# Kernel tuning notes

Hardware: AMD Instinct MI355X
Metric: run time of the kernel (lower is better)

Reference implementation:

```python
import jax, jax.numpy as jnp
import numpy as np

B, IN, U = 16, 1024, 1024


def _wSw(W, S):
    # W: [i,u], S: [b,i,i] -> W^T S W : [b,u,u]
    return jnp.einsum('iu,bij,jv->buv', W, S, W)


def _xSx(x, Wsig):
    # (sum_i x_i^2) * W_Sigma, broadcast over batch
    return jnp.sum(x * x, axis=1)[:, None, None] * Wsig


def _trS(S, Wsig):
    return jnp.trace(S, axis1=1, axis2=2)[:, None, None] * Wsig


def _hadamard_sigma(s1, s2, m1, m2):
    # s1*s2 + diag(m1) s2 diag(m1) + diag(m2) s1 diag(m2)
    return (s1 * s2
            + m1[:, :, None] * s2 * m1[:, None, :]
            + m2[:, :, None] * s1 * m2[:, None, :])


def _act_sigma(g, S):
    # S * outer(g, g)
    return S * (g[:, :, None] * g[:, None, :])


def setup_inputs() -> dict:
    key = jax.random.key(0)
    ks = jax.random.split(key, 16)
    f32 = jnp.float32
    init_mu, ini_sigma = 0.05, -4.6
    inp = {
        'mu_inputs': jax.random.normal(ks[0], (B, IN), f32),
        'sigma_inputs': 0.01 * jax.random.normal(ks[1], (B, IN, IN), f32),
        'prev_state': 0.1 * jax.random.normal(ks[2], (B, U), f32),
        'Sigma_state': 0.01 * jax.random.normal(ks[3], (B, U, U), f32),
        'U_z': init_mu * jax.random.normal(ks[4], (IN, U), f32),
        'uz_sigma': jnp.full((U,), ini_sigma, f32),
        'W_z': init_mu * jax.random.normal(ks[5], (U, U), f32),
        'wz_sigma': jnp.full((U,), ini_sigma, f32),
        'U_r': init_mu * jax.random.normal(ks[6], (IN, U), f32),
        'ur_sigma': jnp.full((U,), ini_sigma, f32),
        'W_r': init_mu * jax.random.normal(ks[7], (U, U), f32),
        'wr_sigma': jnp.full((U,), ini_sigma, f32),
        'U_h': init_mu * jax.random.normal(ks[8], (IN, U), f32),
        'uh_sigma': jnp.full((U,), ini_sigma, f32),
        'W_h': init_mu * jax.random.normal(ks[9], (U, U), f32),
        'wh_sigma': jnp.full((U,), ini_sigma, f32),
    }
    return inp


def reference(mu_inputs, sigma_inputs, prev_state, Sigma_state,
              U_z, uz_sigma, W_z, wz_sigma,
              U_r, ur_sigma, W_r, wr_sigma,
              U_h, uh_sigma, W_h, wh_sigma):
    sp = jax.nn.softplus
    # ---- z gate ----
    pre_z = mu_inputs @ U_z + prev_state @ W_z
    z = jax.nn.sigmoid(pre_z)
    Uz_S, Wz_S = jnp.diag(sp(uz_sigma)), jnp.diag(sp(wz_sigma))
    Sigma_zz = (_wSw(U_z, sigma_inputs) + _xSx(mu_inputs, Uz_S) + _trS(sigma_inputs, Uz_S)
                + _wSw(W_z, Sigma_state) + _xSx(prev_state, Wz_S) + _trS(Sigma_state, Wz_S))
    Sigma_z = _act_sigma(z * (1.0 - z), Sigma_zz)  # analytic d sigmoid
    # ---- r gate ----
    pre_r = mu_inputs @ U_r + prev_state @ W_r
    r = jax.nn.sigmoid(pre_r)
    Ur_S, Wr_S = jnp.diag(sp(ur_sigma)), jnp.diag(sp(wr_sigma))
    Sigma_rr = (_wSw(U_r, sigma_inputs) + _xSx(mu_inputs, Ur_S) + _trS(sigma_inputs, Ur_S)
                + _wSw(W_r, Sigma_state) + _xSx(prev_state, Wr_S) + _trS(Sigma_state, Wr_S))
    Sigma_r = _act_sigma(r * (1.0 - r), Sigma_rr)
    # ---- h gate ----
    sr = prev_state * r
    pre_h = mu_inputs @ U_h + sr @ W_h
    h = jnp.tanh(pre_h)
    Uh_S, Wh_S = jnp.diag(sp(uh_sigma)), jnp.diag(sp(wh_sigma))
    sigma_g = _hadamard_sigma(Sigma_state, Sigma_r, prev_state, r)
    Sigma_hh = (_wSw(U_h, sigma_inputs) + _xSx(mu_inputs, Uh_S) + _trS(sigma_inputs, Uh_S)
                + _wSw(W_h, sigma_g) + _xSx(sr, Wh_S) + _trS(sigma_g, Wh_S))
    Sigma_h = _act_sigma(1.0 - h * h, Sigma_hh)  # analytic d tanh
    # ---- combine ----
    mu_out = z * prev_state + (1.0 - z) * h
    sigma_a = _hadamard_sigma(Sigma_z, Sigma_state, z, prev_state)
    sigma_b = _hadamard_sigma(Sigma_z, Sigma_h, 1.0 - z, h)
    sigma_ab = Sigma_z * (prev_state[:, :, None] * h[:, None, :])
    sigma_abT = Sigma_z * (h[:, :, None] * prev_state[:, None, :])
    Sigma_out = sigma_a + sigma_b - sigma_ab - sigma_abT
    Sigma_out = jnp.where(jnp.isfinite(Sigma_out), Sigma_out, jnp.zeros_like(Sigma_out))
    eye = jnp.eye(Sigma_out.shape[-1], dtype=bool)
    Sigma_out = jnp.where(eye, jnp.abs(Sigma_out), Sigma_out)
    return mu_out, Sigma_out
```

## Files before the change

### kernel.cpp

```cpp
#include <hip/hip_runtime.h>
#include <math.h>


#define B_  16
#define N_  1024
#define NN_ (1024*1024)

typedef __bf16 bf16x8 __attribute__((ext_vector_type(8)));
typedef float  f32x4  __attribute__((ext_vector_type(4)));
typedef unsigned short ushort8v __attribute__((ext_vector_type(8)));

__device__ __forceinline__ unsigned short f2bf(float f) {
  union { float f; unsigned int u; } v; v.f = f;
  unsigned int r = v.u + 0x7fffu + ((v.u >> 16) & 1u);
  return (unsigned short)(r >> 16);
}
__device__ __forceinline__ float bf2f(unsigned short h) {
  union { unsigned int u; float f; } v; v.u = ((unsigned int)h) << 16;
  return v.f;
}
__device__ __forceinline__ float f4get(const float4& v, int q) {
  return q == 0 ? v.x : (q == 1 ? v.y : (q == 2 ? v.z : v.w));
}
__device__ __forceinline__ unsigned short u4get(const ushort4& v, int q) {
  return q == 0 ? v.x : (q == 1 ? v.y : (q == 2 ? v.z : v.w));
}

__device__ __forceinline__ void gload_lds16(const void* g, void* l) {
  __builtin_amdgcn_global_load_lds((__attribute__((address_space(1))) void*)g,
                                   (__attribute__((address_space(3))) void*)l,
                                   16, 0, 0);
}

#define MFMA_ __builtin_amdgcn_mfma_f32_16x16x32_bf16
#define SBAR_()  do { __builtin_amdgcn_sched_barrier(0); \
                      __builtin_amdgcn_s_barrier(); \
                      __builtin_amdgcn_sched_barrier(0); } while (0)

template<int OMODE, int PAIR>
__global__ __launch_bounds__(512)
void gemm8p(const unsigned short* __restrict__ A, int lda, long aStride, int koffA,
            const unsigned short* __restrict__ Bm, const unsigned short* __restrict__ Bm2,
            int ldb, long bStride, int K,
            void* __restrict__ Out, int ldo, long oStride, int noff,
            const float* __restrict__ act,
            const float* __restrict__ spU, const float* __restrict__ spW,
            const float* __restrict__ dU, const float* __restrict__ dW,
            const unsigned short* __restrict__ SzP, const float* __restrict__ SstP,
            const float* __restrict__ zV, const float* __restrict__ prevV,
            const float* __restrict__ hV)
{
  __shared__ __align__(16) char ldsb[131072];
  const int id = blockIdx.x;
  const int xcd = id & 7, rest = id >> 3;
  const int mt = rest & 3, pp = rest >> 2;
  const int panel = xcd + (pp << 3);
  const int nt = panel & 3;
  const int b  = (panel >> 2) & 15;
  const int ps = PAIR ? (panel >> 6) : 0;
  const unsigned short* Bsel = (PAIR && ps) ? Bm2 : Bm;
  const int kofx = koffA + (ps ? 1024 : 0);
  const int nofx = noff  + (ps ? 1024 : 0);
  const int mbase = mt << 8, nbase = nt << 8;
  const int tid = threadIdx.x, lane = tid & 63, w = tid >> 6;
  const int wm = w >> 2, wn = w & 3;
  const int NT = K >> 6;

  f32x4 acc[8][4];
  const f32x4 zero4 = {0.f, 0.f, 0.f, 0.f};
#pragma unroll
  for (int i = 0; i < 8; i++)
#pragma unroll
    for (int j = 0; j < 4; j++) acc[i][j] = zero4;

  const int l3 = lane >> 3, l7 = lane & 7;
  const int posg = l7 ^ l3;
  const int gr = (l3 << 1) + (posg >> 2);
  const int gc = (posg & 3) << 3;
  const int bi0 = w << 1, bi1 = bi0 + 1;
  const int rS0 = ((bi0 >> 1) << 4) + gr, cS0 = ((bi0 & 1) << 5) + gc;
  const int rS1 = ((bi1 >> 1) << 4) + gr, cS1 = ((bi1 & 1) << 5) + gc;
  const unsigned short* Ab = A + (size_t)b * aStride + (size_t)mbase * lda + kofx;
  const unsigned short* Bb = Bsel + (size_t)b * bStride + (size_t)nbase * ldb;
  const int d0 = w << 11, d1 = (w << 11) + 1024;

  auto SA = [&](int tt, int h) {
    char* dst = ldsb + ((tt & 1) << 16) + (h << 14);
    const unsigned short* s = Ab + (size_t)(h << 7) * lda + ((size_t)tt << 6);
    gload_lds16(s + (size_t)rS0 * lda + cS0, dst + d0);
    gload_lds16(s + (size_t)rS1 * lda + cS1, dst + d1);
  };
  auto SB = [&](int tt, int h) {
    char* dst = ldsb + ((tt & 1) << 16) + 32768 + (h << 14);
    const unsigned short* s = Bb + (size_t)(h << 7) * ldb + ((size_t)tt << 6);
    gload_lds16(s + (size_t)rS0 * ldb + cS0, dst + d0);
    gload_lds16(s + (size_t)rS1 * ldb + cS1, dst + d1);
  };

  const int lrow = lane & 15, c4 = lane >> 4;
  const int aoff = ((lrow >> 1) << 7) + (((((lrow & 1) << 2) | c4) ^ (lrow >> 1)) << 4);
  const int abase = wm << 14;
  const int bbase = 32768 + ((wn >> 1) << 14);
  const int brg   = (wn & 1) << 2;
  auto LDA = [&](const char* pb, int mi, int ks) -> bf16x8 {
    return *(const bf16x8*)(pb + abase + (((mi << 1) + ks) << 10) + aoff);
  };
  auto LDB = [&](const char* pb, int ni, int ks) -> bf16x8 {
    return *(const bf16x8*)(pb + bbase + ((((brg + ni) << 1) + ks) << 10) + aoff);
  };

  SA(0, 0); SA(0, 1); SB(0, 0); SB(0, 1);
  if (NT > 1) { SB(1, 0); SB(1, 1); }
  asm volatile("s_waitcnt vmcnt(4)" ::: "memory");
  SBAR_();

  bf16x8 avA[4], avB[4], bvA[4], bvB[4];
#pragma unroll
  for (int i = 0; i < 4; i++) avB[i] = LDA(ldsb, i, 0);
#pragma unroll
  for (int i = 0; i < 4; i++) bvB[i] = LDB(ldsb, i, 0);
  __builtin_amdgcn_sched_barrier(0);

  for (int kt = 0; kt < NT; ++kt) {
    const char* pb = ldsb + ((kt & 1) << 16);
    const char* pn = ldsb + (((kt + 1) & 1) << 16);
#pragma unroll
    for (int i = 0; i < 4; i++) avA[i] = LDA(pb, 4 + i, 0);
    if (kt + 1 < NT) SA(kt + 1, 0);
    SBAR_();
    __builtin_amdgcn_s_setprio(1);
#pragma unroll
    for (int ni = 0; ni < 4; ni++)
#pragma unroll
      for (int mi = 0; mi < 4; mi++)
        acc[mi][ni] = MFMA_(avB[mi], bvB[ni], acc[mi][ni], 0, 0, 0);
    __builtin_amdgcn_s_setprio(0);
    SBAR_();
#pragma unroll
    for (int i = 0; i < 4; i++) avB[i] = LDA(pb, i, 1);
#pragma unroll
    for (int i = 0; i < 4; i++) bvA[i] = LDB(pb, i, 1);
    if (kt + 1 < NT) SA(kt + 1, 1);
    SBAR_();
    __builtin_amdgcn_s_setprio(1);
#pragma unroll
    for (int ni = 0; ni < 4; ni++)
#pragma unroll
      for (int mi = 0; mi < 4; mi++)
        acc[4 + mi][ni] = MFMA_(avA[mi], bvB[ni], acc[4 + mi][ni], 0, 0, 0);
    __builtin_amdgcn_s_setprio(0);
    SBAR_();
#pragma unroll
    for (int i = 0; i < 4; i++) avA[i] = LDA(pb, 4 + i, 1);
    SBAR_();
    __builtin_amdgcn_s_setprio(1);
#pragma unroll
    for (int ni = 0; ni < 4; ni++)
#pragma unroll
      for (int mi = 0; mi < 4; mi++)
        acc[mi][ni] = MFMA_(avB[mi], bvA[ni], acc[mi][ni], 0, 0, 0);
    __builtin_amdgcn_s_setprio(0);
    SBAR_();
    if (kt + 2 < NT) {
      SB(kt + 2, 0); SB(kt + 2, 1);
      asm volatile("s_waitcnt vmcnt(4)" ::: "memory");
    } else if (kt + 1 < NT) {
      asm volatile("s_waitcnt vmcnt(0)" ::: "memory");
    }
    SBAR_();
    if (kt + 1 < NT) {
#pragma unroll
      for (int i = 0; i < 4; i++) avB[i] = LDA(pn, i, 0);
#pragma unroll
      for (int i = 0; i < 4; i++) bvB[i] = LDB(pn, i, 0);
    }
    __builtin_amdgcn_sched_barrier(0);
    __builtin_amdgcn_s_setprio(1);
#pragma unroll
    for (int ni = 0; ni < 4; ni++)
#pragma unroll
      for (int mi = 0; mi < 4; mi++)
        acc[4 + mi][ni] = MFMA_(avA[mi], bvA[ni], acc[4 + mi][ni], 0, 0, 0);
    __builtin_amdgcn_s_setprio(0);
    SBAR_();
  }

  if (OMODE == 2) {
    const float* ghb = act + b * N_;
    const float dUb = dU[b], dWb = dW[b];
    const float* zb = zV + b * N_;
    const float* pv = prevV + b * N_;
    const float* hb = hV + b * N_;
    const unsigned short* SzB = SzP + (size_t)b * NN_;
    const float* SstB = SstP + (size_t)b * NN_;
    float zvv[4], pvv[4], hvv[4], gvv[4];
    int vcol[4];
#pragma unroll
    for (int ni = 0; ni < 4; ni++) {
      const int v = nbase + wn * 64 + ni * 16 + (lane & 15);
      vcol[ni] = v;
      zvv[ni] = zb[v]; pvv[ni] = pv[v]; hvv[ni] = hb[v]; gvv[ni] = ghb[v];
    }
#pragma unroll
    for (int mi = 0; mi < 8; mi++) {
      const int u0 = mbase + wm * 128 + mi * 16 + ((lane >> 4) << 2);
#pragma unroll
      for (int r = 0; r < 4; r++) {
        const int u = u0 + r;
        const float zu = zb[u], pu = pv[u], hu = hb[u], gu = ghb[u];
        const float diag = dUb * spU[u] + dWb * spW[u];
#pragma unroll
        for (int ni = 0; ni < 4; ni++) {
          const int v = vcol[ni];
          float shh = acc[mi][ni][r];
          if (u == v) shh += diag;
          shh *= gu * gvv[ni];
          const float szv = bf2f(SzB[(size_t)u * N_ + v]);
          const float stt = SstB[(size_t)u * N_ + v];
          float res = szv * stt + zu * zvv[ni] * stt + pu * pvv[ni] * szv
                    + szv * shh + (1.f - zu) * (1.f - zvv[ni]) * shh + hu * hvv[ni] * szv
                    - szv * (pu * hvv[ni]) - szv * (hu * pvv[ni]);
          if (!isfinite(res)) res = 0.f;
          if (u == v) res = fabsf(res);
          ((float*)Out)[(size_t)b * oStride + (size_t)u * ldo + v] = res;
        }
      }
    }
  } else {
    __syncthreads();
    unsigned short* scr = (unsigned short*)(ldsb + w * 16384);
    const float* actb = (OMODE == 1) ? (act + b * N_) : nullptr;
    float dUb = 0.f, dWb = 0.f;
    if (OMODE == 1) { dUb = dU[b]; dWb = dW[b]; }
#pragma unroll
    for (int mi = 0; mi < 8; mi++) {
      const int rl0 = mi * 16 + ((lane >> 4) << 2);
#pragma unroll
      for (int ni = 0; ni < 4; ni++) {
        const int cl = ni * 16 + (lane & 15);
#pragma unroll
        for (int r = 0; r < 4; r++) {
          const int rl = rl0 + r;
          float val = acc[mi][ni][r];
          if (OMODE == 1) {
            const int u = mbase + wm * 128 + rl, v = nbase + wn * 64 + cl;
            if (u == v) val += dUb * spU[u] + dWb * spW[u];
            val *= actb[u] * actb[v];
          }
          scr[rl * 64 + ((((cl >> 3) ^ (rl & 7))) << 3) + (cl & 7)] = f2bf(val);
        }
      }
    }
    asm volatile("s_waitcnt lgkmcnt(0)" ::: "memory");
    __builtin_amdgcn_sched_barrier(0);
    unsigned short* ob = (unsigned short*)Out + (size_t)b * oStride
        + (size_t)(mbase + wm * 128) * ldo + nofx + nbase + wn * 64;
#pragma unroll
    for (int pq = 0; pq < 16; pq++) {
      const int row = pq * 8 + (lane >> 3);
      const int ch = (lane & 7) ^ (row & 7);
      ushort8v vv = *(const ushort8v*)&scr[row * 64 + ((lane & 7) << 3)];
      *(ushort8v*)(ob + (size_t)row * ldo + ch * 8) = vv;
    }
  }
}


__global__ void conv_bf16_2(const float* __restrict__ in0, unsigned short* __restrict__ out0,
                            const float* __restrict__ in1, unsigned short* __restrict__ out1,
                            int n4)
{
  const float* in = blockIdx.y ? in1 : in0;
  unsigned short* out = blockIdx.y ? out1 : out0;
  int i = blockIdx.x * 256 + threadIdx.x;
  const int stride = gridDim.x * 256;
  for (; i < n4; i += stride) {
    const float4 v = ((const float4*)in)[i];
    ushort4 o;
    o.x = f2bf(v.x); o.y = f2bf(v.y); o.z = f2bf(v.z); o.w = f2bf(v.w);
    ((ushort4*)out)[i] = o;
  }
}

__global__ void build_AT(const float* __restrict__ Uz, const float* __restrict__ Wz,
                         const float* __restrict__ Ur, const float* __restrict__ Wr,
                         const float* __restrict__ Uh, const float* __restrict__ Wh,
                         unsigned short* __restrict__ AT)
{
  __shared__ float tile[32][33];
  const int g = blockIdx.z;
  const float* U = g == 0 ? Uz : (g == 1 ? Ur : Uh);
  const float* W = g == 0 ? Wz : (g == 1 ? Wr : Wh);
  const int u0  = blockIdx.x * 32;
  const int k0g = blockIdx.y * 32;
  const float* src = (k0g >= 1024) ? W : U;
  const int kloc = k0g & 1023;
  const int tx = threadIdx.x & 31, ty = threadIdx.x >> 5;
  unsigned short* out = AT + (size_t)g * N_ * 2048;
#pragma unroll
  for (int i = 0; i < 32; i += 8) tile[ty + i][tx] = src[(size_t)(kloc + ty + i) * N_ + u0 + tx];
  __syncthreads();
#pragma unroll
  for (int i = 0; i < 32; i += 8)
    out[(size_t)(u0 + ty + i) * 2048 + k0g + tx] = f2bf(tile[tx][ty + i]);
}

__global__ void softplus6(const float* a0, const float* a1, const float* a2,
                          const float* a3, const float* a4, const float* a5,
                          float* __restrict__ sp)
{
  const float* src[6] = {a0, a1, a2, a3, a4, a5};
  const int g = blockIdx.x;
  const float* s = src[g];
  for (int i = threadIdx.x; i < N_; i += 256) {
    float x = s[i];
    sp[g * N_ + i] = (x > 20.f) ? x : log1pf(expf(x));
  }
}

__global__ void scalars1(const float* __restrict__ mu, const float* __restrict__ prev,
                         const float* __restrict__ sin_, const float* __restrict__ Sst,
                         float* __restrict__ dA, float* __restrict__ dBzr)
{
  __shared__ float red[256];
  const int b = blockIdx.x;
  float s1 = 0.f, s2 = 0.f;
  for (int i = threadIdx.x; i < N_; i += 256) {
    const float m = mu[b * N_ + i];
    s1 += m * m + sin_[(size_t)b * NN_ + (size_t)i * (N_ + 1)];
    const float p = prev[b * N_ + i];
    s2 += p * p + Sst[(size_t)b * NN_ + (size_t)i * (N_ + 1)];
  }
  red[threadIdx.x] = s1; __syncthreads();
  for (int s = 128; s > 0; s >>= 1) { if (threadIdx.x < s) red[threadIdx.x] += red[threadIdx.x + s]; __syncthreads(); }
  if (threadIdx.x == 0) dA[b] = red[0];
  __syncthreads();
  red[threadIdx.x] = s2; __syncthreads();
  for (int s = 128; s > 0; s >>= 1) { if (threadIdx.x < s) red[threadIdx.x] += red[threadIdx.x + s]; __syncthreads(); }
  if (threadIdx.x == 0) dBzr[b] = red[0];
}

__global__ __launch_bounds__(256)
void gate_pre2(const float* __restrict__ x1, const float* __restrict__ x2,
               const float* __restrict__ U0, const float* __restrict__ W0,
               const float* __restrict__ U1, const float* __restrict__ W1,
               float* __restrict__ Ppart)
{
  const int g  = blockIdx.z;
  const int ks = blockIdx.y;
  const int out = blockIdx.x * 256 + threadIdx.x;
  const int b = out >> 10, col = out & 1023;
  const float* x = (ks < 4) ? x1 : x2;
  const float* Wm = (g == 0) ? ((ks < 4) ? U0 : W0) : ((ks < 4) ? U1 : W1);
  const int k0 = (ks & 3) * 256;
  const float* xb = x + b * N_ + k0;
  const float* wp = Wm + (size_t)k0 * N_ + col;
  float acc = 0.f;
#pragma unroll 8
  for (int k = 0; k < 256; k++)
    acc += xb[k] * wp[(size_t)k * N_];
  Ppart[(g * 8 + ks) * (B_ * N_) + out] = acc;
}

__global__ void gate_act2(const float* __restrict__ P,
                          float* __restrict__ z, float* __restrict__ gz,
                          float* __restrict__ r, float* __restrict__ gr)
{
  const int out = blockIdx.x * 256 + threadIdx.x;
  float a0 = 0.f, a1 = 0.f;
#pragma unroll
  for (int ks = 0; ks < 8; ks++) {
    a0 += P[ks * (B_ * N_) + out];
    a1 += P[(8 + ks) * (B_ * N_) + out];
  }
  const float s0 = 1.f / (1.f + expf(-a0));
  const float s1 = 1.f / (1.f + expf(-a1));
  z[out] = s0; gz[out] = s0 * (1.f - s0);
  r[out] = s1; gr[out] = s1 * (1.f - s1);
}

__global__ __launch_bounds__(256)
void gate_pre1(const float* __restrict__ x1, const float* __restrict__ x2,
               const float* __restrict__ U0, const float* __restrict__ W0,
               float* __restrict__ Ppart)
{
  const int ks = blockIdx.y;
  const int out = blockIdx.x * 256 + threadIdx.x;
  const int b = out >> 10, col = out & 1023;
  const float* x = (ks < 4) ? x1 : x2;
  const float* Wm = (ks < 4) ? U0 : W0;
  const int k0 = (ks & 3) * 256;
  const float* xb = x + b * N_ + k0;
  const float* wp = Wm + (size_t)k0 * N_ + col;
  float acc = 0.f;
#pragma unroll 8
  for (int k = 0; k < 256; k++)
    acc += xb[k] * wp[(size_t)k * N_];
  Ppart[ks * (B_ * N_) + out] = acc;
}

__global__ void gate_act1(const float* __restrict__ P,
                          const float* __restrict__ z, const float* __restrict__ prev,
                          float* __restrict__ h, float* __restrict__ gh,
                          float* __restrict__ mu_out)
{
  const int out = blockIdx.x * 256 + threadIdx.x;
  float a0 = 0.f;
#pragma unroll
  for (int ks = 0; ks < 8; ks++) a0 += P[ks * (B_ * N_) + out];
  const float s = tanhf(a0);
  h[out] = s; gh[out] = 1.f - s * s;
  const float zz = z[out];
  mu_out[out] = zz * prev[out] + (1.f - zz) * s;
}

__global__ void sr_csr(const float* __restrict__ prev, const float* __restrict__ r,
                       float* __restrict__ sr, float* __restrict__ csr)
{
  __shared__ float red[256];
  const int b = blockIdx.x;
  float s = 0.f;
  for (int i = threadIdx.x; i < N_; i += 256) {
    const float v = prev[b * N_ + i] * r[b * N_ + i];
    sr[b * N_ + i] = v;
    s += v * v;
  }
  red[threadIdx.x] = s; __syncthreads();
  for (int k = 128; k > 0; k >>= 1) { if (threadIdx.x < k) red[threadIdx.x] += red[threadIdx.x + k]; __syncthreads(); }
  if (threadIdx.x == 0) csr[b] = red[0];
}

__global__ void hadamard_sg(const unsigned short* __restrict__ SstH,
                            unsigned short* __restrict__ Sg,
                            const float* __restrict__ prev, const float* __restrict__ r)
{
  const size_t idx = ((size_t)blockIdx.x * 256 + threadIdx.x) * 4;
  const int b = (int)(idx >> 20);
  const int rem = (int)(idx & (NN_ - 1));
  const int i = rem >> 10, j0 = rem & 1023;
  const float pi = prev[b * N_ + i], ri = r[b * N_ + i];
  const ushort4 ss4 = *(const ushort4*)(SstH + (size_t)b * NN_ + rem);
  const ushort4 sr4 = *(const ushort4*)(Sg + (size_t)b * NN_ + rem);
  ushort4 o;
  unsigned short* op = (unsigned short*)&o;
#pragma unroll
  for (int q = 0; q < 4; q++) {
    const float srv = bf2f(u4get(sr4, q));
    const float stv = bf2f(u4get(ss4, q));
    const float pj = prev[b * N_ + j0 + q];
    const float rj = r[b * N_ + j0 + q];
    op[q] = f2bf(stv * srv + pi * pj * srv + ri * rj * stv);
  }
  *(ushort4*)(Sg + (size_t)b * NN_ + rem) = o;
}

__global__ void scalars2(const unsigned short* __restrict__ Sg,
                         const float* __restrict__ csr, float* __restrict__ dBh)
{
  __shared__ float red[256];
  const int b = blockIdx.x;
  float s = 0.f;
  for (int i = threadIdx.x; i < N_; i += 256)
    s += bf2f(Sg[(size_t)b * NN_ + (size_t)i * (N_ + 1)]);
  red[threadIdx.x] = s; __syncthreads();
  for (int k = 128; k > 0; k >>= 1) { if (threadIdx.x < k) red[threadIdx.x] += red[threadIdx.x + k]; __syncthreads(); }
  if (threadIdx.x == 0) dBh[b] = red[0] + csr[b];
}


extern "C" void kernel_launch(void* const* d_in, const int* in_sizes, int n_in,
                              void* d_out, int out_size, void* d_ws, size_t ws_size,
                              hipStream_t stream)
{
  const float* mu   = (const float*)d_in[0];
  const float* sin_ = (const float*)d_in[1];
  const float* prev = (const float*)d_in[2];
  const float* Sst  = (const float*)d_in[3];
  const float* Uz = (const float*)d_in[4];  const float* uzs = (const float*)d_in[5];
  const float* Wz = (const float*)d_in[6];  const float* wzs = (const float*)d_in[7];
  const float* Ur = (const float*)d_in[8];  const float* urs = (const float*)d_in[9];
  const float* Wr = (const float*)d_in[10]; const float* wrs = (const float*)d_in[11];
  const float* Uh = (const float*)d_in[12]; const float* uhs = (const float*)d_in[13];
  const float* Wh = (const float*)d_in[14]; const float* whs = (const float*)d_in[15];

  char* ws = (char*)d_ws;
  size_t off = 0;
  auto take = [&](size_t bytes) -> char* {
    char* p = ws + off;
    off = (off + bytes + 255) & ~(size_t)255;
    return p;
  };
  unsigned short* Tcm = (unsigned short*)take((size_t)B_ * 2048 * 1024 * 2);
  unsigned short* Sz  = (unsigned short*)take((size_t)B_ * NN_ * 2);
  unsigned short* Sg  = (unsigned short*)take((size_t)B_ * NN_ * 2);
  unsigned short* AT  = (unsigned short*)take((size_t)3 * N_ * 2048 * 2);
  float* Ppart = (float*)take((size_t)16 * B_ * N_ * 4);
  float* sp   = (float*)take(6 * N_ * 4);
  float* z    = (float*)take(B_ * N_ * 4);
  float* gz   = (float*)take(B_ * N_ * 4);
  float* rr   = (float*)take(B_ * N_ * 4);
  float* gr   = (float*)take(B_ * N_ * 4);
  float* h    = (float*)take(B_ * N_ * 4);
  float* gh   = (float*)take(B_ * N_ * 4);
  float* sr   = (float*)take(B_ * N_ * 4);
  float* dA   = (float*)take(64);
  float* dBzr = (float*)take(64);
  float* dBh  = (float*)take(64);
  float* csr  = (float*)take(64);
  if (off > ws_size) return;

  float* mu_out = (float*)d_out;
  float* SigOut = (float*)d_out + (size_t)B_ * N_;
  unsigned short* SinH = (unsigned short*)SigOut;
  unsigned short* SstH = (unsigned short*)SigOut + (size_t)B_ * NN_;

  const unsigned short* ATz = AT;
  const unsigned short* ATr = AT + (size_t)N_ * 2048;
  const unsigned short* ATh = AT + (size_t)2 * N_ * 2048;

  conv_bf16_2<<<dim3(2048, 2), 256, 0, stream>>>(sin_, SinH, Sst, SstH, B_ * NN_ / 4);
  softplus6<<<6, 256, 0, stream>>>(uzs, wzs, urs, wrs, uhs, whs, sp);
  scalars1<<<16, 256, 0, stream>>>(mu, prev, sin_, Sst, dA, dBzr);
  build_AT<<<dim3(32, 64, 3), 256, 0, stream>>>(Uz, Wz, Ur, Wr, Uh, Wh, AT);
  gate_pre2<<<dim3(64, 8, 2), 256, 0, stream>>>(mu, prev, Uz, Wz, Ur, Wr, Ppart);
  gate_act2<<<64, 256, 0, stream>>>(Ppart, z, gz, rr, gr);
  sr_csr<<<16, 256, 0, stream>>>(prev, rr, sr, csr);
  gate_pre1<<<dim3(64, 8), 256, 0, stream>>>(mu, sr, Uh, Wh, Ppart);
  gate_act1<<<64, 256, 0, stream>>>(Ppart, z, prev, h, gh, mu_out);

  const long tS = (long)2048 * 1024;

  gemm8p<0, 1><<<512, 512, 0, stream>>>(ATz, 2048, 0, 0, SinH, SstH, 1024, (long)NN_, 1024,
                                        Tcm, 2048, tS, 0, nullptr, nullptr, nullptr, nullptr, nullptr,
                                        nullptr, nullptr, nullptr, nullptr, nullptr);
  gemm8p<1, 0><<<256, 512, 0, stream>>>(ATz, 2048, 0, 0, Tcm, nullptr, 2048, tS, 2048,
                                        Sz, 1024, (long)NN_, 0, gz, sp + 0, sp + 1024, dA, dBzr,
                                        nullptr, nullptr, nullptr, nullptr, nullptr);
  gemm8p<0, 1><<<512, 512, 0, stream>>>(ATr, 2048, 0, 0, SinH, SstH, 1024, (long)NN_, 1024,
                                        Tcm, 2048, tS, 0, nullptr, nullptr, nullptr, nullptr, nullptr,
                                        nullptr, nullptr, nullptr, nullptr, nullptr);
  gemm8p<1, 0><<<256, 512, 0, stream>>>(ATr, 2048, 0, 0, Tcm, nullptr, 2048, tS, 2048,
                                        Sg, 1024, (long)NN_, 0, gr, sp + 2048, sp + 3072, dA, dBzr,
                                        nullptr, nullptr, nullptr, nullptr, nullptr);
  hadamard_sg<<<16384, 256, 0, stream>>>(SstH, Sg, prev, rr);
  scalars2<<<16, 256, 0, stream>>>(Sg, csr, dBh);
  gemm8p<0, 1><<<512, 512, 0, stream>>>(ATh, 2048, 0, 0, SinH, Sg, 1024, (long)NN_, 1024,
                                        Tcm, 2048, tS, 0, nullptr, nullptr, nullptr, nullptr, nullptr,
                                        nullptr, nullptr, nullptr, nullptr, nullptr);
  gemm8p<2, 0><<<256, 512, 0, stream>>>(ATh, 2048, 0, 0, Tcm, nullptr, 2048, tS, 2048,
                                        SigOut, 1024, (long)NN_, 0, gh, sp + 4096, sp + 5120, dA, dBh,
                                        Sz, Sst, z, prev, h);
}
```

Baseline: 547.8 us.

## Fuse Hadamard sigma_g into r-gate GEMM epilogue and vectorize final epilogue

Adds an OMODE 3 epilogue to the second-stage r-gate GEMM that applies the Hadamard combination with Sigma_state, prev and r directly before writing Sg. This removes the separate hadamard_sg kernel and its extra read and write pass over a 16x1024x1024 bf16 tensor. The OMODE 2 final epilogue is also moved to go through the LDS swizzle, so it does 8-wide vector loads and stores instead of strided scalar accesses. In exchange the Sigma_hh accumulator is now rounded to bf16 before the final combine, which adds precision loss.

```diff
diff --git a/kernel.cpp b/kernel.cpp
--- a/kernel.cpp
+++ b/kernel.cpp
@@ -18,12 +18,6 @@
 __device__ __forceinline__ float bf2f(unsigned short h) {
   union { unsigned int u; float f; } v; v.u = ((unsigned int)h) << 16;
   return v.f;
-}
-__device__ __forceinline__ float f4get(const float4& v, int q) {
-  return q == 0 ? v.x : (q == 1 ? v.y : (q == 2 ? v.z : v.w));
-}
-__device__ __forceinline__ unsigned short u4get(const ushort4& v, int q) {
-  return q == 0 ? v.x : (q == 1 ? v.y : (q == 2 ? v.z : v.w));
 }
 
 __device__ __forceinline__ void gload_lds16(const void* g, void* l) {
@@ -185,82 +179,98 @@
     SBAR_();
   }
 
-  if (OMODE == 2) {
-    const float* ghb = act + b * N_;
-    const float dUb = dU[b], dWb = dW[b];
-    const float* zb = zV + b * N_;
-    const float* pv = prevV + b * N_;
-    const float* hb = hV + b * N_;
-    const unsigned short* SzB = SzP + (size_t)b * NN_;
-    const float* SstB = SstP + (size_t)b * NN_;
-    float zvv[4], pvv[4], hvv[4], gvv[4];
-    int vcol[4];
+  __syncthreads();
+  unsigned short* scr = (unsigned short*)(ldsb + w * 16384);
+  const float* actb = act ? (act + b * N_) : nullptr;
+  float dUb = 0.f, dWb = 0.f;
+  if (OMODE != 0) { dUb = dU[b]; dWb = dW[b]; }
+
+#pragma unroll
+  for (int mi = 0; mi < 8; mi++) {
+    const int rl0 = mi * 16 + ((lane >> 4) << 2);
 #pragma unroll
     for (int ni = 0; ni < 4; ni++) {
-      const int v = nbase + wn * 64 + ni * 16 + (lane & 15);
-      vcol[ni] = v;
-      zvv[ni] = zb[v]; pvv[ni] = pv[v]; hvv[ni] = hb[v]; gvv[ni] = ghb[v];
-    }
-#pragma unroll
-    for (int mi = 0; mi < 8; mi++) {
-      const int u0 = mbase + wm * 128 + mi * 16 + ((lane >> 4) << 2);
+      const int cl = ni * 16 + (lane & 15);
 #pragma unroll
       for (int r = 0; r < 4; r++) {
-        const int u = u0 + r;
-        const float zu = zb[u], pu = pv[u], hu = hb[u], gu = ghb[u];
-        const float diag = dUb * spU[u] + dWb * spW[u];
-#pragma unroll
-        for (int ni = 0; ni < 4; ni++) {
-          const int v = vcol[ni];
-          float shh = acc[mi][ni][r];
-          if (u == v) shh += diag;
-          shh *= gu * gvv[ni];
-          const float szv = bf2f(SzB[(size_t)u * N_ + v]);
-          const float stt = SstB[(size_t)u * N_ + v];
-          float res = szv * stt + zu * zvv[ni] * stt + pu * pvv[ni] * szv
-                    + szv * shh + (1.f - zu) * (1.f - zvv[ni]) * shh + hu * hvv[ni] * szv
-                    - szv * (pu * hvv[ni]) - szv * (hu * pvv[ni]);
-          if (!isfinite(res)) res = 0.f;
-          if (u == v) res = fabsf(res);
-          ((float*)Out)[(size_t)b * oStride + (size_t)u * ldo + v] = res;
+        const int rl = rl0 + r;
+        float val = acc[mi][ni][r];
+        if (OMODE != 0) {
+          const int u = mbase + wm * 128 + rl, v = nbase + wn * 64 + cl;
+          if (u == v) val += dUb * spU[u] + dWb * spW[u];
+          val *= actb[u] * actb[v];
         }
+        scr[rl * 64 + ((((cl >> 3) ^ (rl & 7))) << 3) + (cl & 7)] = f2bf(val);
       }
     }
-  } else {
-    __syncthreads();
-    unsigned short* scr = (unsigned short*)(ldsb + w * 16384);
-    const float* actb = (OMODE == 1) ? (act + b * N_) : nullptr;
-    float dUb = 0.f, dWb = 0.f;
-    if (OMODE == 1) { dUb = dU[b]; dWb = dW[b]; }
-#pragma unroll
-    for (int mi = 0; mi < 8; mi++) {
-      const int rl0 = mi * 16 + ((lane >> 4) << 2);
-#pragma unroll
-      for (int ni = 0; ni < 4; ni++) {
-        const int cl = ni * 16 + (lane & 15);
-#pragma unroll
-        for (int r = 0; r < 4; r++) {
-          const int rl = rl0 + r;
-          float val = acc[mi][ni][r];
-          if (OMODE == 1) {
-            const int u = mbase + wm * 128 + rl, v = nbase + wn * 64 + cl;
-            if (u == v) val += dUb * spU[u] + dWb * spW[u];
-            val *= actb[u] * actb[v];
-          }
-          scr[rl * 64 + ((((cl >> 3) ^ (rl & 7))) << 3) + (cl & 7)] = f2bf(val);
-        }
+  }
+  asm volatile("s_waitcnt lgkmcnt(0)" ::: "memory");
+  __builtin_amdgcn_sched_barrier(0);
+
+#pragma unroll
+  for (int pq = 0; pq < 16; pq++) {
+    const int row = pq * 8 + (lane >> 3);
+    const int slot = lane & 7;
+    const int ch = slot ^ (row & 7);
+    const int u = mbase + wm * 128 + row;
+    const int v0 = nbase + wn * 64 + (ch << 3);
+    ushort8v s8 = *(const ushort8v*)&scr[row * 64 + (slot << 3)];
+    if (OMODE == 0 || OMODE == 1) {
+      unsigned short* ob = (unsigned short*)Out + (size_t)b * oStride
+                         + (size_t)u * ldo + nofx + v0;
+      *(ushort8v*)ob = s8;
+    } else if (OMODE == 3) {
+      const float pu = prevV[b * N_ + u];
+      const float ru = zV[b * N_ + u];
+      const ushort8v st8 = *(const ushort8v*)(SzP + (size_t)b * NN_ + (size_t)u * N_ + v0);
+      const f32x4 pv0 = *(const f32x4*)(prevV + b * N_ + v0);
+      const f32x4 pv1 = *(const f32x4*)(prevV + b * N_ + v0 + 4);
+      const f32x4 rv0 = *(const f32x4*)(zV + b * N_ + v0);
+      const f32x4 rv1 = *(const f32x4*)(zV + b * N_ + v0 + 4);
+      ushort8v o8;
+#pragma unroll
+      for (int q = 0; q < 8; q++) {
+        const float srv = bf2f((unsigned short)s8[q]);
+        const float stt = bf2f((unsigned short)st8[q]);
+        const float pv = (q < 4) ? pv0[q] : pv1[q - 4];
+        const float rv = (q < 4) ? rv0[q] : rv1[q - 4];
+        o8[q] = f2bf(stt * srv + pu * pv * srv + ru * rv * stt);
       }
-    }
-    asm volatile("s_waitcnt lgkmcnt(0)" ::: "memory");
-    __builtin_amdgcn_sched_barrier(0);
-    unsigned short* ob = (unsigned short*)Out + (size_t)b * oStride
-        + (size_t)(mbase + wm * 128) * ldo + nofx + nbase + wn * 64;
-#pragma unroll
-    for (int pq = 0; pq < 16; pq++) {
-      const int row = pq * 8 + (lane >> 3);
-      const int ch = (lane & 7) ^ (row & 7);
-      ushort8v vv = *(const ushort8v*)&scr[row * 64 + ((lane & 7) << 3)];
-      *(ushort8v*)(ob + (size_t)row * ldo + ch * 8) = vv;
+      unsigned short* ob = (unsigned short*)Out + (size_t)b * oStride
+                         + (size_t)u * ldo + v0;
+      *(ushort8v*)ob = o8;
+    } else {
+      const float zu = zV[b * N_ + u];
+      const float pu = prevV[b * N_ + u];
+      const float hu = hV[b * N_ + u];
+      const ushort8v sz8 = *(const ushort8v*)(SzP + (size_t)b * NN_ + (size_t)u * N_ + v0);
+      const f32x4 st0 = *(const f32x4*)(SstP + (size_t)b * NN_ + (size_t)u * N_ + v0);
+      const f32x4 st1 = *(const f32x4*)(SstP + (size_t)b * NN_ + (size_t)u * N_ + v0 + 4);
+      const f32x4 zv0 = *(const f32x4*)(zV + b * N_ + v0);
+      const f32x4 zv1 = *(const f32x4*)(zV + b * N_ + v0 + 4);
+      const f32x4 pv0 = *(const f32x4*)(prevV + b * N_ + v0);
+      const f32x4 pv1 = *(const f32x4*)(prevV + b * N_ + v0 + 4);
+      const f32x4 hv0 = *(const f32x4*)(hV + b * N_ + v0);
+      const f32x4 hv1 = *(const f32x4*)(hV + b * N_ + v0 + 4);
+      f32x4 o0, o1;
+#pragma unroll
+      for (int q = 0; q < 8; q++) {
+        const float shh = bf2f((unsigned short)s8[q]);
+        const float szv = bf2f((unsigned short)sz8[q]);
+        const float stt = (q < 4) ? st0[q] : st1[q - 4];
+        const float zv  = (q < 4) ? zv0[q] : zv1[q - 4];
+        const float pv  = (q < 4) ? pv0[q] : pv1[q - 4];
+        const float hv  = (q < 4) ? hv0[q] : hv1[q - 4];
+        float res = szv * stt + zu * zv * stt + pu * pv * szv
+                  + szv * shh + (1.f - zu) * (1.f - zv) * shh + hu * hv * szv
+                  - szv * (pu * hv) - szv * (hu * pv);
+        if (!isfinite(res)) res = 0.f;
+        if (u == v0 + q) res = fabsf(res);
+        if (q < 4) o0[q] = res; else o1[q - 4] = res;
+      }
+      float* ob = (float*)Out + (size_t)b * oStride + (size_t)u * ldo + v0;
+      *(f32x4*)ob = o0;
+      *(f32x4*)(ob + 4) = o1;
     }
   }
 }
@@ -428,30 +438,6 @@
   red[threadIdx.x] = s; __syncthreads();
   for (int k = 128; k > 0; k >>= 1) { if (threadIdx.x < k) red[threadIdx.x] += red[threadIdx.x + k]; __syncthreads(); }
   if (threadIdx.x == 0) csr[b] = red[0];
-}
-
-__global__ void hadamard_sg(const unsigned short* __restrict__ SstH,
-                            unsigned short* __restrict__ Sg,
-                            const float* __restrict__ prev, const float* __restrict__ r)
-{
-  const size_t idx = ((size_t)blockIdx.x * 256 + threadIdx.x) * 4;
-  const int b = (int)(idx >> 20);
-  const int rem = (int)(idx & (NN_ - 1));
-  const int i = rem >> 10, j0 = rem & 1023;
-  const float pi = prev[b * N_ + i], ri = r[b * N_ + i];
-  const ushort4 ss4 = *(const ushort4*)(SstH + (size_t)b * NN_ + rem);
-  const ushort4 sr4 = *(const ushort4*)(Sg + (size_t)b * NN_ + rem);
-  ushort4 o;
-  unsigned short* op = (unsigned short*)&o;
-#pragma unroll
-  for (int q = 0; q < 4; q++) {
-    const float srv = bf2f(u4get(sr4, q));
-    const float stv = bf2f(u4get(ss4, q));
-    const float pj = prev[b * N_ + j0 + q];
-    const float rj = r[b * N_ + j0 + q];
-    op[q] = f2bf(stv * srv + pi * pj * srv + ri * rj * stv);
-  }
-  *(ushort4*)(Sg + (size_t)b * NN_ + rem) = o;
 }
 
 __global__ void scalars2(const unsigned short* __restrict__ Sg,
@@ -539,10 +525,9 @@
   gemm8p<0, 1><<<512, 512, 0, stream>>>(ATr, 2048, 0, 0, SinH, SstH, 1024, (long)NN_, 1024,
                                         Tcm, 2048, tS, 0, nullptr, nullptr, nullptr, nullptr, nullptr,
                                         nullptr, nullptr, nullptr, nullptr, nullptr);
-  gemm8p<1, 0><<<256, 512, 0, stream>>>(ATr, 2048, 0, 0, Tcm, nullptr, 2048, tS, 2048,
+  gemm8p<3, 0><<<256, 512, 0, stream>>>(ATr, 2048, 0, 0, Tcm, nullptr, 2048, tS, 2048,
                                         Sg, 1024, (long)NN_, 0, gr, sp + 2048, sp + 3072, dA, dBzr,
-                                        nullptr, nullptr, nullptr, nullptr, nullptr);
-  hadamard_sg<<<16384, 256, 0, stream>>>(SstH, Sg, prev, rr);
+                                        SstH, nullptr, rr, prev, nullptr);
   scalars2<<<16, 256, 0, stream>>>(Sg, csr, dBh);
   gemm8p<0, 1><<<512, 512, 0, stream>>>(ATh, 2048, 0, 0, SinH, Sg, 1024, (long)NN_, 1024,
                                         Tcm, 2048, tS, 0, nullptr, nullptr, nullptr, nullptr, nullptr,
```

New measurement: 539.3 us. About the same (-1.6%).
